# Optimization experiments

Measured on AMD Instinct MI355X. Metric: run time of the kernel, lower is better.

## Reference

```python
import jax, jax.numpy as jnp
import numpy as np

GRID_NUM = 28
IMG_SIZE = 224.0
GRID_SIZE = IMG_SIZE / GRID_NUM
LAMBDA_COORD = 5.0
LAMBDA_NOOBJ = 0.5
NUM_CLASSES = 20
EPS = 1e-12


def setup_inputs() -> dict:
    key = jax.random.key(0)
    k1, k2, k3 = jax.random.split(key, 3)
    B, S = 1024, GRID_NUM
    y_pred = jax.random.uniform(k1, (B, S, S, 30), dtype=jnp.float32)
    # y_true channel 0: class id in {0..20}; 0 means no object. channels 1:5: (x, y, w, h)
    cls = jax.random.randint(k2, (B, S, S, 1), 0, NUM_CLASSES + 1).astype(jnp.float32)
    box = jax.random.uniform(k3, (B, S, S, 4), dtype=jnp.float32)
    y_true = jnp.concatenate([cls, box], axis=-1)
    return {"y_pred": y_pred, "y_true": y_true}


def _corners(box, gi, gj):
    # box[..., 0:2] are cell-relative center offsets, box[..., 2:4] are image-relative w/h
    cx = (gj + box[..., 0]) * GRID_SIZE
    cy = (gi + box[..., 1]) * GRID_SIZE
    w = box[..., 2] * IMG_SIZE
    h = box[..., 3] * IMG_SIZE
    return cx - w / 2, cy - h / 2, cx + w / 2, cy + h / 2


def _iou(box_a, box_b, gi, gj):
    ax1, ay1, ax2, ay2 = _corners(box_a, gi, gj)
    bx1, by1, bx2, by2 = _corners(box_b, gi, gj)
    iw = jnp.maximum(jnp.minimum(ax2, bx2) - jnp.maximum(ax1, bx1), 0.0)
    ih = jnp.maximum(jnp.minimum(ay2, by2) - jnp.maximum(ay1, by1), 0.0)
    inter = iw * ih
    area_a = jnp.maximum(ax2 - ax1, 0.0) * jnp.maximum(ay2 - ay1, 0.0)
    area_b = jnp.maximum(bx2 - bx1, 0.0) * jnp.maximum(by2 - by1, 0.0)
    return inter / (area_a + area_b - inter + EPS)


def reference(y_pred, y_true):
    B, S = y_pred.shape[0], y_pred.shape[1]
    gi = jnp.arange(S, dtype=jnp.float32)[None, :, None]  # broadcast over (B, S, S)
    gj = jnp.arange(S, dtype=jnp.float32)[None, None, :]

    obj_mask = y_true[..., 0] != 0.0  # (B, S, S)
    true_box = y_true[..., 1:5]

    iou0 = _iou(y_pred[..., 0:4], true_box, gi, gj)
    iou1 = _iou(y_pred[..., 5:9], true_box, gi, gj)
    # original: choose 0 iff iou0 > iou1, else 1
    choose1 = ~(iou0 > iou1)

    conf_pred = jnp.where(choose1, y_pred[..., 9], y_pred[..., 4])
    conf_true = jnp.where(choose1, iou1, iou0)
    xy_pred = jnp.where(choose1[..., None], y_pred[..., 5:7], y_pred[..., 0:2])

    loss_conf_obj = jnp.square(conf_pred - conf_true)
    loss_coord = LAMBDA_COORD * jnp.sum(jnp.square(xy_pred - y_true[..., 1:3]), axis=-1)

    cls_idx = y_true[..., 0].astype(jnp.int32) - 1
    cls_onehot = jax.nn.one_hot(cls_idx, NUM_CLASSES, dtype=y_pred.dtype)
    loss_cls = jnp.sum(jnp.square(y_pred[..., 10:] - cls_onehot), axis=-1)

    loss_conf_noobj = LAMBDA_NOOBJ * (jnp.square(y_pred[..., 4]) + jnp.square(y_pred[..., 9]))

    bsz = jnp.float32(B)
    loss_confidence = jnp.sum(jnp.where(obj_mask, loss_conf_obj, loss_conf_noobj)) / bsz
    loss_coordinate = jnp.sum(jnp.where(obj_mask, loss_coord, 0.0)) / bsz
    loss_classification = jnp.sum(jnp.where(obj_mask, loss_cls, 0.0)) / bsz
    return loss_confidence + loss_coordinate + loss_classification
```

## Files before the change

kernel.cpp:

```cpp
#include <hip/hip_runtime.h>


#define S_GRID 28
#define N_CELLS (1024 * S_GRID * S_GRID)
#define CPW 64
#define WPB 4
#define BLOCK (WPB * 64)
#define N_WAVES (N_CELLS / CPW)
#define NBLOCKS (N_WAVES / WPB)

__device__ __forceinline__ float iou_calc(float bx, float by, float bw, float bh,
                                          float tx, float ty, float tw, float th,
                                          float gi, float gj) {
    float acx = (gj + bx) * 8.0f;
    float acy = (gi + by) * 8.0f;
    float aw  = bw * 224.0f;
    float ah  = bh * 224.0f;
    float ax1 = acx - aw * 0.5f, ax2 = acx + aw * 0.5f;
    float ay1 = acy - ah * 0.5f, ay2 = acy + ah * 0.5f;
    float bcx = (gj + tx) * 8.0f;
    float bcy = (gi + ty) * 8.0f;
    float btw = tw * 224.0f;
    float bth = th * 224.0f;
    float bx1 = bcx - btw * 0.5f, bx2 = bcx + btw * 0.5f;
    float by1 = bcy - bth * 0.5f, by2 = bcy + bth * 0.5f;

    float iw = fmaxf(fminf(ax2, bx2) - fmaxf(ax1, bx1), 0.0f);
    float ih = fmaxf(fminf(ay2, by2) - fmaxf(ay1, by1), 0.0f);
    float inter = iw * ih;
    float area_a = fmaxf(ax2 - ax1, 0.0f) * fmaxf(ay2 - ay1, 0.0f);
    float area_b = fmaxf(bx2 - bx1, 0.0f) * fmaxf(by2 - by1, 0.0f);
    return inter / (area_a + area_b - inter + 1e-12f);
}

__global__ __launch_bounds__(BLOCK, 4) void yolo_loss_kernel(const float2* __restrict__ yp2,
                                                             const float* __restrict__ yt,
                                                             float* __restrict__ partials) {
    __shared__ float sp[WPB][CPW * 30];

    int tid  = threadIdx.x;
    int lane = tid & 63;
    int wave = tid >> 6;
    int gwave = blockIdx.x * WPB + wave;

    const float2* pb = yp2 + (size_t)gwave * (CPW * 30 / 2);
    float2 v[15];
#pragma unroll
    for (int k = 0; k < 15; ++k) v[k] = pb[k * 64 + lane];

    float2* spw2 = (float2*)sp[wave];
#pragma unroll
    for (int k = 0; k < 15; ++k) spw2[k * 64 + lane] = v[k];

    int cell = gwave * CPW + lane;
    const float* t = yt + (size_t)cell * 5;
    float tc = t[0], tx = t[1], ty = t[2], tw = t[3], th = t[4];

    float pr[30];
    const float* p = sp[wave] + lane * 30;
#pragma unroll
    for (int k = 0; k < 30; ++k) pr[k] = p[k];

    int ij = cell % (S_GRID * S_GRID);
    float gi = (float)(ij / S_GRID);
    float gj = (float)(ij % S_GRID);

    float iou0 = iou_calc(pr[0], pr[1], pr[2], pr[3], tx, ty, tw, th, gi, gj);
    float iou1 = iou_calc(pr[5], pr[6], pr[7], pr[8], tx, ty, tw, th, gi, gj);
    bool choose1 = !(iou0 > iou1);

    float conf_pred = choose1 ? pr[9] : pr[4];
    float conf_true = choose1 ? iou1 : iou0;
    float xp = choose1 ? pr[5] : pr[0];
    float yp = choose1 ? pr[6] : pr[1];

    float dcf = conf_pred - conf_true;
    float d0 = xp - tx, d1 = yp - ty;

    int cls = (int)tc - 1;
    float lcls = 0.0f;
#pragma unroll
    for (int k = 0; k < 20; ++k) {
        float oh = (k == cls) ? 1.0f : 0.0f;
        float d = pr[10 + k] - oh;
        lcls += d * d;
    }

    float obj_loss   = dcf * dcf + 5.0f * (d0 * d0 + d1 * d1) + lcls;
    float noobj_loss = 0.5f * (pr[4] * pr[4] + pr[9] * pr[9]);
    float val = (tc != 0.0f) ? obj_loss : noobj_loss;

#pragma unroll
    for (int off = 32; off > 0; off >>= 1) {
        val += __shfl_down(val, off, 64);
    }
    if (lane == 0) partials[gwave] = val;
}

__global__ __launch_bounds__(256) void reduce_kernel(const float* __restrict__ partials,
                                                     float* __restrict__ out) {
    int tid = threadIdx.x;
    float s = 0.0f;
#pragma unroll
    for (int k = 0; k < 49; ++k) {
        s += partials[k * 256 + tid];
    }
#pragma unroll
    for (int off = 32; off > 0; off >>= 1) {
        s += __shfl_down(s, off, 64);
    }
    __shared__ float wsum[4];
    int lane = tid & 63;
    int wid  = tid >> 6;
    if (lane == 0) wsum[wid] = s;
    __syncthreads();
    if (tid == 0) {
        out[0] = (wsum[0] + wsum[1] + wsum[2] + wsum[3]) * (1.0f / 1024.0f);
    }
}

extern "C" void kernel_launch(void* const* d_in, const int* in_sizes, int n_in,
                              void* d_out, int out_size, void* d_ws, size_t ws_size,
                              hipStream_t stream) {
    const float2* y_pred = (const float2*)d_in[0];
    const float*  y_true = (const float*)d_in[1];
    float* out = (float*)d_out;
    float* partials = (float*)d_ws;

    yolo_loss_kernel<<<NBLOCKS, BLOCK, 0, stream>>>(y_pred, y_true, partials);
    reduce_kernel<<<1, 256, 0, stream>>>(partials, out);
}
```

Baseline: 151.1 us.

## Convert loss kernel to persistent grid-stride loop with register prefetch

The kernel now launches a fixed 1024 blocks. Each wave loops over multiple 64-cell tiles and accumulates its loss in a register, and it prefetches the next tile's y_pred and y_true values into registers while the current tile is computed. This is meant to hide global memory latency inside each wave and to shrink the partials array and the final reduction. It raises register pressure, and the fixed block count may lower occupancy compared with the original many-block launch.

```diff
diff --git a/kernel.cpp b/kernel.cpp
--- a/kernel.cpp
+++ b/kernel.cpp
@@ -4,10 +4,11 @@
 #define S_GRID 28
 #define N_CELLS (1024 * S_GRID * S_GRID)
 #define CPW 64
+#define NT (N_CELLS / CPW)
 #define WPB 4
 #define BLOCK (WPB * 64)
-#define N_WAVES (N_CELLS / CPW)
-#define NBLOCKS (N_WAVES / WPB)
+#define NBLOCKS 1024
+#define TOTW (NBLOCKS * WPB)
 
 __device__ __forceinline__ float iou_calc(float bx, float by, float bw, float bh,
                                           float tx, float ty, float tw, float th,
@@ -33,68 +34,87 @@
     return inter / (area_a + area_b - inter + 1e-12f);
 }
 
-__global__ __launch_bounds__(BLOCK, 4) void yolo_loss_kernel(const float2* __restrict__ yp2,
-                                                             const float* __restrict__ yt,
-                                                             float* __restrict__ partials) {
+__global__ __launch_bounds__(BLOCK) void yolo_loss_kernel(const float2* __restrict__ yp2,
+                                                          const float* __restrict__ yt,
+                                                          float* __restrict__ partials) {
     __shared__ float sp[WPB][CPW * 30];
 
     int tid  = threadIdx.x;
     int lane = tid & 63;
     int wave = tid >> 6;
-    int gwave = blockIdx.x * WPB + wave;
+    int wid  = blockIdx.x * WPB + wave;
 
-    const float2* pb = yp2 + (size_t)gwave * (CPW * 30 / 2);
+    float acc = 0.0f;
+
     float2 v[15];
+    float t5[5];
+    {
+        const float2* pb = yp2 + (size_t)wid * (CPW * 30 / 2);
 #pragma unroll
-    for (int k = 0; k < 15; ++k) v[k] = pb[k * 64 + lane];
+        for (int k = 0; k < 15; ++k) v[k] = pb[k * 64 + lane];
+        const float* tt = yt + ((size_t)wid * CPW + lane) * 5;
+#pragma unroll
+        for (int k = 0; k < 5; ++k) t5[k] = tt[k];
+    }
 
     float2* spw2 = (float2*)sp[wave];
+
+    for (int t = wid; t < NT; t += TOTW) {
 #pragma unroll
-    for (int k = 0; k < 15; ++k) spw2[k * 64 + lane] = v[k];
+        for (int k = 0; k < 15; ++k) spw2[k * 64 + lane] = v[k];
+        float tc = t5[0], tx = t5[1], ty = t5[2], tw = t5[3], th = t5[4];
 
-    int cell = gwave * CPW + lane;
-    const float* t = yt + (size_t)cell * 5;
-    float tc = t[0], tx = t[1], ty = t[2], tw = t[3], th = t[4];
+        int tn = t + TOTW;
+        if (tn < NT) {
+            const float2* pbn = yp2 + (size_t)tn * (CPW * 30 / 2);
+#pragma unroll
+            for (int k = 0; k < 15; ++k) v[k] = pbn[k * 64 + lane];
+            const float* ttn = yt + ((size_t)tn * CPW + lane) * 5;
+#pragma unroll
+            for (int k = 0; k < 5; ++k) t5[k] = ttn[k];
+        }
 
-    float pr[30];
-    const float* p = sp[wave] + lane * 30;
+        int cell = t * CPW + lane;
+        int ij = cell % (S_GRID * S_GRID);
+        float gi = (float)(ij / S_GRID);
+        float gj = (float)(ij % S_GRID);
+
+        float pr[30];
+        const float* p = sp[wave] + lane * 30;
 #pragma unroll
-    for (int k = 0; k < 30; ++k) pr[k] = p[k];
+        for (int k = 0; k < 30; ++k) pr[k] = p[k];
 
-    int ij = cell % (S_GRID * S_GRID);
-    float gi = (float)(ij / S_GRID);
-    float gj = (float)(ij % S_GRID);
+        float iou0 = iou_calc(pr[0], pr[1], pr[2], pr[3], tx, ty, tw, th, gi, gj);
+        float iou1 = iou_calc(pr[5], pr[6], pr[7], pr[8], tx, ty, tw, th, gi, gj);
+        bool choose1 = !(iou0 > iou1);
 
-    float iou0 = iou_calc(pr[0], pr[1], pr[2], pr[3], tx, ty, tw, th, gi, gj);
-    float iou1 = iou_calc(pr[5], pr[6], pr[7], pr[8], tx, ty, tw, th, gi, gj);
-    bool choose1 = !(iou0 > iou1);
+        float conf_pred = choose1 ? pr[9] : pr[4];
+        float conf_true = choose1 ? iou1 : iou0;
+        float xp = choose1 ? pr[5] : pr[0];
+        float yp = choose1 ? pr[6] : pr[1];
 
-    float conf_pred = choose1 ? pr[9] : pr[4];
-    float conf_true = choose1 ? iou1 : iou0;
-    float xp = choose1 ? pr[5] : pr[0];
-    float yp = choose1 ? pr[6] : pr[1];
+        float dcf = conf_pred - conf_true;
+        float d0 = xp - tx, d1 = yp - ty;
 
-    float dcf = conf_pred - conf_true;
-    float d0 = xp - tx, d1 = yp - ty;
+        int cls = (int)tc - 1;
+        float lcls = 0.0f;
+#pragma unroll
+        for (int k = 0; k < 20; ++k) {
+            float oh = (k == cls) ? 1.0f : 0.0f;
+            float d = pr[10 + k] - oh;
+            lcls += d * d;
+        }
 
-    int cls = (int)tc - 1;
-    float lcls = 0.0f;
-#pragma unroll
-    for (int k = 0; k < 20; ++k) {
-        float oh = (k == cls) ? 1.0f : 0.0f;
-        float d = pr[10 + k] - oh;
-        lcls += d * d;
+        float obj_loss   = dcf * dcf + 5.0f * (d0 * d0 + d1 * d1) + lcls;
+        float noobj_loss = 0.5f * (pr[4] * pr[4] + pr[9] * pr[9]);
+        acc += (tc != 0.0f) ? obj_loss : noobj_loss;
     }
-
-    float obj_loss   = dcf * dcf + 5.0f * (d0 * d0 + d1 * d1) + lcls;
-    float noobj_loss = 0.5f * (pr[4] * pr[4] + pr[9] * pr[9]);
-    float val = (tc != 0.0f) ? obj_loss : noobj_loss;
 
 #pragma unroll
     for (int off = 32; off > 0; off >>= 1) {
-        val += __shfl_down(val, off, 64);
+        acc += __shfl_down(acc, off, 64);
     }
-    if (lane == 0) partials[gwave] = val;
+    if (lane == 0) partials[wid] = acc;
 }
 
 __global__ __launch_bounds__(256) void reduce_kernel(const float* __restrict__ partials,
@@ -102,7 +122,7 @@
     int tid = threadIdx.x;
     float s = 0.0f;
 #pragma unroll
-    for (int k = 0; k < 49; ++k) {
+    for (int k = 0; k < 16; ++k) {
         s += partials[k * 256 + tid];
     }
 #pragma unroll
```

Measured after the change: 153.5 us. About the same (+1.6%).

## Split each cell across two lanes and use algebraic class-loss expansion

Applied to the files above, without the earlier changes.

Each wave now handles 32 cells, with two lanes per cell each reading half of the 30 prediction channels from LDS. The class loss is rewritten as sum of squares minus 2·p[cls] plus 1, combined across the lane pair with a shuffle. This halves per-lane register and LDS-read load and doubles the number of waves, with higher occupancy requested via launch bounds. In exchange, the reduction kernel sums twice as many partials, and half the lanes sit idle during the IoU math.

```diff
diff --git a/kernel.cpp b/kernel.cpp
--- a/kernel.cpp
+++ b/kernel.cpp
@@ -3,11 +3,11 @@
 
 #define S_GRID 28
 #define N_CELLS (1024 * S_GRID * S_GRID)
-#define CPW 64
+#define CPT 32
+#define NT2 (N_CELLS / CPT)
 #define WPB 4
 #define BLOCK (WPB * 64)
-#define N_WAVES (N_CELLS / CPW)
-#define NBLOCKS (N_WAVES / WPB)
+#define NBLOCKS (NT2 / WPB)
 
 __device__ __forceinline__ float iou_calc(float bx, float by, float bw, float bh,
                                           float tx, float ty, float tw, float th,
@@ -33,86 +33,111 @@
     return inter / (area_a + area_b - inter + 1e-12f);
 }
 
-__global__ __launch_bounds__(BLOCK, 4) void yolo_loss_kernel(const float2* __restrict__ yp2,
+__global__ __launch_bounds__(BLOCK, 8) void yolo_loss_kernel(const float2* __restrict__ yp2,
                                                              const float* __restrict__ yt,
                                                              float* __restrict__ partials) {
-    __shared__ float sp[WPB][CPW * 30];
+    __shared__ float sp[WPB][CPT * 30];
 
-    int tid  = threadIdx.x;
-    int lane = tid & 63;
-    int wave = tid >> 6;
-    int gwave = blockIdx.x * WPB + wave;
+    int tid   = threadIdx.x;
+    int lane  = tid & 63;
+    int wave  = tid >> 6;
+    int tile  = blockIdx.x * WPB + wave;
+    int qcell = lane >> 1;
+    int half  = lane & 1;
+    int cell  = tile * CPT + qcell;
 
-    const float2* pb = yp2 + (size_t)gwave * (CPW * 30 / 2);
-    float2 v[15];
+    const float2* pb = yp2 + (size_t)tile * (CPT * 30 / 2);
+    float2* spw = (float2*)sp[wave];
 #pragma unroll
-    for (int k = 0; k < 15; ++k) v[k] = pb[k * 64 + lane];
-
-    float2* spw2 = (float2*)sp[wave];
-#pragma unroll
-    for (int k = 0; k < 15; ++k) spw2[k * 64 + lane] = v[k];
-
-    int cell = gwave * CPW + lane;
-    const float* t = yt + (size_t)cell * 5;
-    float tc = t[0], tx = t[1], ty = t[2], tw = t[3], th = t[4];
-
-    float pr[30];
-    const float* p = sp[wave] + lane * 30;
-#pragma unroll
-    for (int k = 0; k < 30; ++k) pr[k] = p[k];
-
-    int ij = cell % (S_GRID * S_GRID);
-    float gi = (float)(ij / S_GRID);
-    float gj = (float)(ij % S_GRID);
-
-    float iou0 = iou_calc(pr[0], pr[1], pr[2], pr[3], tx, ty, tw, th, gi, gj);
-    float iou1 = iou_calc(pr[5], pr[6], pr[7], pr[8], tx, ty, tw, th, gi, gj);
-    bool choose1 = !(iou0 > iou1);
-
-    float conf_pred = choose1 ? pr[9] : pr[4];
-    float conf_true = choose1 ? iou1 : iou0;
-    float xp = choose1 ? pr[5] : pr[0];
-    float yp = choose1 ? pr[6] : pr[1];
-
-    float dcf = conf_pred - conf_true;
-    float d0 = xp - tx, d1 = yp - ty;
-
-    int cls = (int)tc - 1;
-    float lcls = 0.0f;
-#pragma unroll
-    for (int k = 0; k < 20; ++k) {
-        float oh = (k == cls) ? 1.0f : 0.0f;
-        float d = pr[10 + k] - oh;
-        lcls += d * d;
+    for (int k = 0; k < 8; ++k) {
+        int idx = k * 64 + lane;
+        if (idx < 480) spw[idx] = pb[idx];
     }
 
-    float obj_loss   = dcf * dcf + 5.0f * (d0 * d0 + d1 * d1) + lcls;
-    float noobj_loss = 0.5f * (pr[4] * pr[4] + pr[9] * pr[9]);
-    float val = (tc != 0.0f) ? obj_loss : noobj_loss;
+    int base_f = qcell * 30 + half * 15;
+    const float*  spf  = sp[wave];
+    const float2* spf2 = (const float2*)sp[wave];
+    int f2s = (base_f + 1) >> 1;
+    float s[15];
+    {
+        float2 r[7];
+#pragma unroll
+        for (int j = 0; j < 7; ++j) r[j] = spf2[f2s + j];
+        float rs = spf[half ? base_f : base_f + 14];
+        if (half == 0) {
+#pragma unroll
+            for (int j = 0; j < 7; ++j) { s[2 * j] = r[j].x; s[2 * j + 1] = r[j].y; }
+            s[14] = rs;
+        } else {
+            s[0] = rs;
+#pragma unroll
+            for (int j = 0; j < 7; ++j) { s[1 + 2 * j] = r[j].x; s[2 + 2 * j] = r[j].y; }
+        }
+    }
+
+    float csum = 0.0f;
+#pragma unroll
+    for (int j = 0; j < 15; ++j) {
+        bool inc = (half != 0) || (j >= 10);
+        float q = inc ? s[j] : 0.0f;
+        csum = fmaf(q, q, csum);
+    }
+    float csum_tot = csum + __shfl_down(csum, 1, 64);
+
+    float val = 0.0f;
+    if (half == 0) {
+        const float* t = yt + (size_t)cell * 5;
+        float tc = t[0], tx = t[1], ty = t[2], tw = t[3], th = t[4];
+
+        int ij = cell % (S_GRID * S_GRID);
+        float gi = (float)(ij / S_GRID);
+        float gj = (float)(ij % S_GRID);
+
+        float iou0 = iou_calc(s[0], s[1], s[2], s[3], tx, ty, tw, th, gi, gj);
+        float iou1 = iou_calc(s[5], s[6], s[7], s[8], tx, ty, tw, th, gi, gj);
+        bool choose1 = !(iou0 > iou1);
+
+        float conf_pred = choose1 ? s[9] : s[4];
+        float conf_true = choose1 ? iou1 : iou0;
+        float xpred = choose1 ? s[5] : s[0];
+        float ypred = choose1 ? s[6] : s[1];
+
+        float dcf = conf_pred - conf_true;
+        float d0 = xpred - tx, d1 = ypred - ty;
+
+        int cls = (int)tc - 1;
+        int cidx = cls < 0 ? 0 : cls;
+        float pcls = spf[qcell * 30 + 10 + cidx];
+        float lcls = csum_tot - 2.0f * pcls + 1.0f;
+
+        float obj_loss   = dcf * dcf + 5.0f * (d0 * d0 + d1 * d1) + lcls;
+        float noobj_loss = 0.5f * (s[4] * s[4] + s[9] * s[9]);
+        val = (tc != 0.0f) ? obj_loss : noobj_loss;
+    }
 
 #pragma unroll
     for (int off = 32; off > 0; off >>= 1) {
         val += __shfl_down(val, off, 64);
     }
-    if (lane == 0) partials[gwave] = val;
+    if (lane == 0) partials[tile] = val;
 }
 
 __global__ __launch_bounds__(256) void reduce_kernel(const float* __restrict__ partials,
                                                      float* __restrict__ out) {
     int tid = threadIdx.x;
-    float s = 0.0f;
+    float ssum = 0.0f;
 #pragma unroll
-    for (int k = 0; k < 49; ++k) {
-        s += partials[k * 256 + tid];
+    for (int k = 0; k < 98; ++k) {
+        ssum += partials[k * 256 + tid];
     }
 #pragma unroll
     for (int off = 32; off > 0; off >>= 1) {
-        s += __shfl_down(s, off, 64);
+        ssum += __shfl_down(ssum, off, 64);
     }
     __shared__ float wsum[4];
     int lane = tid & 63;
     int wid  = tid >> 6;
-    if (lane == 0) wsum[wid] = s;
+    if (lane == 0) wsum[wid] = ssum;
     __syncthreads();
     if (tid == 0) {
         out[0] = (wsum[0] + wsum[1] + wsum[2] + wsum[3]) * (1.0f / 1024.0f);
@@ -122,11 +147,11 @@
 extern "C" void kernel_launch(void* const* d_in, const int* in_sizes, int n_in,
                               void* d_out, int out_size, void* d_ws, size_t ws_size,
                               hipStream_t stream) {
-    const float2* y_pred = (const float2*)d_in[0];
-    const float*  y_true = (const float*)d_in[1];
+    const float2* y_pred2 = (const float2*)d_in[0];
+    const float*  y_true  = (const float*)d_in[1];
     float* out = (float*)d_out;
     float* partials = (float*)d_ws;
 
-    yolo_loss_kernel<<<NBLOCKS, BLOCK, 0, stream>>>(y_pred, y_true, partials);
+    yolo_loss_kernel<<<NBLOCKS, BLOCK, 0, stream>>>(y_pred2, y_true, partials);
     reduce_kernel<<<1, 256, 0, stream>>>(partials, out);
 }
```

Result: no change. 152.7 us (+1.1%).
